# Performance work log

Hardware: AMD Instinct MI355X
Metric: run time of the kernel (lower is better)

The kernel has to match this reference:

```python
import jax, jax.numpy as jnp
import numpy as np

L_MAX = 5
C_IN = 24
HIDDEN = 32
BATCH = 256


def _valid_pairs(l):
    return [(l1, l2) for l1 in range(L_MAX + 1) for l2 in range(L_MAX + 1)
            if abs(l1 - l2) <= l <= l1 + l2]


def _make_cg():
    # Packed padded CG coefficient tensor cg[l1, l2, l, m, m1, m2].
    # Values are fixed deterministic constants; sparsity follows the true
    # selection rule m = m1 + m2 (indices stored shifted by +l).
    D = 2 * L_MAX + 1
    rng = np.random.RandomState(42)
    cg = np.zeros((L_MAX + 1, L_MAX + 1, L_MAX + 1, D, D, D), dtype=np.float32)
    for l in range(L_MAX + 1):
        for (l1, l2) in _valid_pairs(l):
            m = np.arange(-l, l + 1)[:, None, None]
            m1 = np.arange(-l1, l1 + 1)[None, :, None]
            m2 = np.arange(-l2, l2 + 1)[None, None, :]
            mask = (m == m1 + m2).astype(np.float32)
            vals = rng.randn(2 * l + 1, 2 * l1 + 1, 2 * l2 + 1).astype(np.float32)
            cg[l1, l2, l, :2 * l + 1, :2 * l1 + 1, :2 * l2 + 1] = vals * mask
    return jnp.asarray(cg)


def setup_inputs() -> dict:
    key = jax.random.key(0)
    keys = jax.random.split(key, 12)
    inp = {}
    for l in range(L_MAX + 1):
        inp[f"x{l}"] = jax.random.normal(keys[l], (BATCH, C_IN, 2 * l + 1), dtype=jnp.float32)
    for l in range(L_MAX + 1):
        k_in = len(_valid_pairs(l)) * C_IN * C_IN
        scale = 1.0 / np.sqrt(k_in)
        inp[f"W{l}"] = jax.random.normal(keys[6 + l], (HIDDEN, k_in), dtype=jnp.float32) * scale
    inp["cg"] = _make_cg()
    return inp


def reference(x0, x1, x2, x3, x4, x5, W0, W1, W2, W3, W4, W5, cg):
    xs = [x0, x1, x2, x3, x4, x5]
    Ws = [W0, W1, W2, W3, W4, W5]
    outs = []
    for l in range(L_MAX + 1):
        feats = []
        for (l1, l2) in _valid_pairs(l):
            c = cg[l1, l2, l, :2 * l + 1, :2 * l1 + 1, :2 * l2 + 1]  # [2l+1, 2l1+1, 2l2+1]
            # P[b, c1, c2, m] = sum_{m1,m2} cg[m,m1,m2] x_l1[b,c1,m1] x_l2[b,c2,m2]
            p = jnp.einsum('mij,bci,bdj->bcdm', c, xs[l1], xs[l2])
            feats.append(p.reshape(p.shape[0], -1, 2 * l + 1))
        cat = jnp.concatenate(feats, axis=1)  # [B, n_pairs*C*C, 2l+1]
        outs.append(jnp.einsum('hk,bkm->bhm', Ws[l], cat))  # [B, HIDDEN, 2l+1]
    # concat orders along the m axis -> [B, HIDDEN, sum_l (2l+1) = 36]
    return jnp.concatenate(outs, axis=-1)
```

## Files before the change

kernel.cpp:

```cpp
#include <hip/hip_runtime.h>
#include <hip/hip_bf16.h>

typedef __attribute__((ext_vector_type(8))) short bf16x8;
typedef __attribute__((ext_vector_type(4))) float f32x4;
typedef __attribute__((ext_vector_type(2))) float f32x2;

struct Params {
  const float* x[6];
  const float* W[6];
  const float* cg;
  float* out;
  unsigned short* Wb;
};

constexpr int NPAIRS_C[6] = {6, 15, 21, 24, 24, 21};
constexpr int POFF_C[6]   = {0, 6, 21, 42, 66, 90};
constexpr size_t WBASE_C[6] = {0, 110592, 387072, 774144, 1216512, 1658880};
constexpr int KL_C[6]   = {3456, 8640, 12096, 13824, 13824, 12096};
constexpr int LOFF_C[6] = {0, 1, 4, 9, 16, 25};

constexpr int TL1[111] = {
  0,1,2,3,4,5,
  0,1,1,1,2,2,2,3,3,3,4,4,4,5,5,
  0,1,1,1,2,2,2,2,2,3,3,3,3,3,4,4,4,4,5,5,5,
  0,1,1,1,2,2,2,2,2,3,3,3,3,3,3,4,4,4,4,4,5,5,5,5,
  0,1,1,1,2,2,2,2,3,3,3,3,3,4,4,4,4,4,4,5,5,5,5,5,
  0,1,1,2,2,2,3,3,3,3,4,4,4,4,4,5,5,5,5,5,5
};
constexpr int TL2R[111] = {
  0,1,2,3,4,5,
  1,0,1,2,1,2,3,2,3,4,3,4,5,4,5,
  2,1,2,3,0,1,2,3,4,1,2,3,4,5,2,3,4,5,3,4,5,
  3,2,3,4,1,2,3,4,5,0,1,2,3,4,5,1,2,3,4,5,2,3,4,5,
  4,3,4,5,2,3,4,5,1,2,3,4,5,0,1,2,3,4,5,1,2,3,4,5,
  5,4,5,3,4,5,2,3,4,5,1,2,3,4,5,0,1,2,3,4,5
};

__constant__ int c_l1[111] = {
  0,1,2,3,4,5,
  0,1,1,1,2,2,2,3,3,3,4,4,4,5,5,
  0,1,1,1,2,2,2,2,2,3,3,3,3,3,4,4,4,4,5,5,5,
  0,1,1,1,2,2,2,2,2,3,3,3,3,3,3,4,4,4,4,4,5,5,5,5,
  0,1,1,1,2,2,2,2,3,3,3,3,3,4,4,4,4,4,4,5,5,5,5,5,
  0,1,1,2,2,2,3,3,3,3,4,4,4,4,4,5,5,5,5,5,5
};
__constant__ int c_l2[111] = {
  0,1,2,3,4,5,
  1,0,1,2,1,2,3,2,3,4,3,4,5,4,5,
  2,1,2,3,0,1,2,3,4,1,2,3,4,5,2,3,4,5,3,4,5,
  3,2,3,4,1,2,3,4,5,0,1,2,3,4,5,1,2,3,4,5,2,3,4,5,
  4,3,4,5,2,3,4,5,1,2,3,4,5,0,1,2,3,4,5,1,2,3,4,5,
  5,4,5,3,4,5,2,3,4,5,1,2,3,4,5,0,1,2,3,4,5
};
__constant__ int c_mb_l[21]  = {5,5,5,5,5,5, 4,4,4,4,4, 3,3,3,3, 2,2,2, 1,1, 0};
__constant__ int c_mb_m0[21] = {0,2,4,6,8,10, 0,2,4,6,8, 0,2,4,6, 0,2,4, 0,2, 0};
__constant__ int c_GA[9] = {0,1,2,6,7,8,12,13,14};

template<int L>
__device__ __forceinline__ void swz(const Params& P, int u8) {
  constexpr int KL = KL_C[L];
  constexpr int KL8 = KL / 8;
  if (u8 >= 32 * KL8) return;
  const int h  = u8 / KL8;
  const int k  = (u8 - h * KL8) * 8;
  const int pair = k / 576;
  const int kin  = k - pair * 576;
  const int kc = kin >> 5;
  const int g  = (kin >> 3) & 3;
  const float* src = P.W[L] + (size_t)h * KL + k;
  f32x4 v0 = *(const f32x4*)src;
  f32x4 v1 = *(const f32x4*)(src + 4);
  union { __hip_bfloat162 h2; unsigned int u; } z;
  unsigned int o0, o1, o2, o3;
  z.h2 = __float22bfloat162_rn(make_float2(v0.x, v0.y)); o0 = z.u;
  z.h2 = __float22bfloat162_rn(make_float2(v0.z, v0.w)); o1 = z.u;
  z.h2 = __float22bfloat162_rn(make_float2(v1.x, v1.y)); o2 = z.u;
  z.h2 = __float22bfloat162_rn(make_float2(v1.z, v1.w)); o3 = z.u;
  const size_t dst = WBASE_C[L] + (size_t)pair * 18432 + kc * 1024 + (h >> 4) * 512
                   + ((size_t)(g * 16 + (h & 15))) * 8;
  *(uint4*)(P.Wb + dst) = make_uint4(o0, o1, o2, o3);
}

__global__ __launch_bounds__(256)
void swizzle_W(Params P) {
  const int u8 = blockIdx.x * 256 + threadIdx.x;
  switch (blockIdx.y) {
    case 0: swz<0>(P, u8); break;
    case 1: swz<1>(P, u8); break;
    case 2: swz<2>(P, u8); break;
    case 3: swz<3>(P, u8); break;
    case 4: swz<4>(P, u8); break;
    default: swz<5>(P, u8); break;
  }
}

#define XALL_F 0
#define CG_F   7056
#define RED_F  7632
#define SMEM_FLOATS 9680

template<int L>
__device__ __forceinline__ void body(const Params& P, const int mp0, const int btile) {
  constexpr int NP  = NPAIRS_C[L];
  constexpr int OFF = POFF_C[L];
  extern __shared__ float smem[];
  float* xall  = smem + XALL_F;
  float* cgall = smem + CG_F;
  float* red   = smem + RED_F;

  const int t    = threadIdx.x;
  const int lane = t & 63;
  const int w    = t >> 6;
  const int q8   = lane >> 4;
  const int rI   = lane & 15;
  const int b    = rI & 7;
  const int mpL  = rI >> 3;
  const int b0   = btile * 8;

#pragma unroll
  for (int l = 0; l < 6; ++l) {
    const int n = 2 * l + 1;
    const float* src = P.x[l] + (size_t)b0 * 24 * n;
    const int tot = 8 * 24 * n;
    for (int e = t; e < tot; e += 256) {
      const int bc = e / n;
      const int i  = e - bc * n;
      xall[(LOFF_C[l] + i) * 196 + bc] = src[e];
    }
  }
  for (int e = t; e < 2 * NP * 12; e += 256) {
    const int i  = e % 12;
    const int r  = e / 12;
    const int pi = r % NP;
    const int mL = r / NP;
    const int l1 = c_l1[OFF + pi], l2 = c_l2[OFF + pi];
    const int mp = mp0 + mL;
    const int j  = mp + l1 + l2 - L - i;
    float v = 0.f;
    if (mp <= 2 * L && i <= 2 * l1 && j >= 0 && j <= 2 * l2)
      v = P.cg[((size_t)(((l1 * 6 + l2) * 6 + L) * 11 + mp) * 11 + i) * 11 + j];
    cgall[(mL * NP + pi) * 12 + i] = v;
  }
  __syncthreads();

  f32x4 accC0 = {0.f, 0.f, 0.f, 0.f};
  f32x4 accC1 = {0.f, 0.f, 0.f, 0.f};
  const int colb = b * 24;

  for (int g = w; g < 9; g += 4) {
    const int kcA = c_GA[g];
    const int k0  = kcA * 32 + q8 * 8;
    const int cA  = k0 / 24;
    const int d0  = k0 - cA * 24;
    const float* x2base = xall + colb + d0;
    const float* x1base = xall + colb + cA;

#pragma unroll
    for (int pi = 0; pi < NP; ++pi) {
      constexpr int dummy = 0; (void)dummy;
      const int l1 = TL1[OFF + pi], l2 = TL2R[OFF + pi];
      const int n1 = 2 * l1 + 1, n2 = 2 * l2 + 1;
      const int R1 = LOFF_C[l1], R2 = LOFF_C[l2];
      const int mK0w = mp0 + l1 + l2 - L;
      const int mK0l = mK0w + mpL;
      const int i0 = (mK0w - (n2 - 1)) > 0 ? (mK0w - (n2 - 1)) : 0;
      const int i1 = (n1 - 1) < (mK0w + 1) ? (n1 - 1) : (mK0w + 1);

      const unsigned short* wbp = P.Wb + WBASE_C[L] + (size_t)pi * 18432 + lane * 8;
      const bf16x8 wfA0 = *(const bf16x8*)(wbp + kcA * 1024);
      const bf16x8 wfA1 = *(const bf16x8*)(wbp + kcA * 1024 + 512);
      const bf16x8 wfB0 = *(const bf16x8*)(wbp + (kcA + 3) * 1024);
      const bf16x8 wfB1 = *(const bf16x8*)(wbp + (kcA + 3) * 1024 + 512);

      f32x2 pA[4], pB[4];
#pragma unroll
      for (int dd = 0; dd < 4; ++dd) { pA[dd] = (f32x2){0.f, 0.f}; pB[dd] = (f32x2){0.f, 0.f}; }

      const float* cgp = cgall + (mpL * NP + pi) * 12;
      for (int i = i0; i <= i1; ++i) {
        const float cgv = cgp[i];
        int j = mK0l - i;
        j = j < 0 ? 0 : (j > n2 - 1 ? n2 - 1 : j);
        const float* x2p = x2base + (R2 + j) * 196;
        f32x2 xv[4];
        *(f32x4*)&xv[0] = *(const f32x4*)x2p;
        *(f32x4*)&xv[2] = *(const f32x4*)(x2p + 4);
        const float* x1p = x1base + (R1 + i) * 196;
        const float sA = cgv * x1p[0];
        const float sB = cgv * x1p[4];
        const f32x2 svA = {sA, sA}, svB = {sB, sB};
#pragma unroll
        for (int dd = 0; dd < 4; ++dd) {
          pA[dd] += svA * xv[dd];
          pB[dd] += svB * xv[dd];
        }
      }
      union { unsigned int u[4]; bf16x8 v; } zA, zB;
#pragma unroll
      for (int dd = 0; dd < 4; ++dd) {
        union { __hip_bfloat162 h2; unsigned int u; } z;
        z.h2 = __float22bfloat162_rn(make_float2(pA[dd].x, pA[dd].y)); zA.u[dd] = z.u;
        z.h2 = __float22bfloat162_rn(make_float2(pB[dd].x, pB[dd].y)); zB.u[dd] = z.u;
      }
      accC0 = __builtin_amdgcn_mfma_f32_16x16x32_bf16(zA.v, wfA0, accC0, 0, 0, 0);
      accC0 = __builtin_amdgcn_mfma_f32_16x16x32_bf16(zB.v, wfB0, accC0, 0, 0, 0);
      accC1 = __builtin_amdgcn_mfma_f32_16x16x32_bf16(zA.v, wfA1, accC1, 0, 0, 0);
      accC1 = __builtin_amdgcn_mfma_f32_16x16x32_bf16(zB.v, wfB1, accC1, 0, 0, 0);
    }
  }

  {
    const int col16 = lane & 15;
    const int rbase = (w * 16 + (lane >> 4) * 4);
#pragma unroll
    for (int r = 0; r < 4; ++r) {
      red[(rbase + r) * 32 + col16]      = accC0[r];
      red[(rbase + r) * 32 + 16 + col16] = accC1[r];
    }
  }
  __syncthreads();
#pragma unroll
  for (int it = 0; it < 2; ++it) {
    const int idx = t + 256 * it;
    const int row = idx >> 5, h = idx & 31;
    const float v = red[row * 32 + h] + red[512 + row * 32 + h]
                  + red[1024 + row * 32 + h] + red[1536 + row * 32 + h];
    const int ob = row & 7, omL = row >> 3;
    const int mp = mp0 + omL;
    if (mp <= 2 * L)
      P.out[(size_t)(b0 + ob) * 1152 + h * 36 + L * L + mp] = v;
  }
}

__global__ __launch_bounds__(256, 4)
void CGLayer_main(Params P) {
  const int mb = blockIdx.x;
  const int l = c_mb_l[mb], mp0 = c_mb_m0[mb];
  const int btile = blockIdx.y;
  switch (l) {
    case 0: body<0>(P, mp0, btile); break;
    case 1: body<1>(P, mp0, btile); break;
    case 2: body<2>(P, mp0, btile); break;
    case 3: body<3>(P, mp0, btile); break;
    case 4: body<4>(P, mp0, btile); break;
    default: body<5>(P, mp0, btile); break;
  }
}

extern "C" void kernel_launch(void* const* d_in, const int* in_sizes, int n_in,
                              void* d_out, int out_size, void* d_ws, size_t ws_size,
                              hipStream_t stream) {
  Params P;
  for (int i = 0; i < 6; ++i) P.x[i] = (const float*)d_in[i];
  for (int i = 0; i < 6; ++i) P.W[i] = (const float*)d_in[6 + i];
  P.cg  = (const float*)d_in[12];
  P.out = (float*)d_out;
  P.Wb  = (unsigned short*)d_ws;

  dim3 sg(216, 6);
  swizzle_W<<<sg, 256, 0, stream>>>(P);
  dim3 grid(21, 32);
  CGLayer_main<<<grid, 256, SMEM_FLOATS * sizeof(float), stream>>>(P);
}
```

Measured before the change: 168.3 us.

## Drop W swizzle kernel, convert fp32 weights inline, use 9 waves per block

Removes the separate swizzle kernel that converted W to a bf16 MFMA-friendly layout in workspace. The main kernel now reads fp32 W directly from the input and converts it to bf16 in registers before each MFMA. Blocks grow to 576 threads, so each of the 9 k-chunk groups gets its own wave instead of 4 waves looping over them, and the reduction sums over 9 partial buffers. This saves one launch and the workspace write/read, but doubles weight load bytes per MFMA and adds conversion work in the hot loop. The larger reduction buffer also raises shared memory per block.

```diff
diff --git a/kernel.cpp b/kernel.cpp
--- a/kernel.cpp
+++ b/kernel.cpp
@@ -10,12 +10,10 @@
   const float* W[6];
   const float* cg;
   float* out;
-  unsigned short* Wb;
 };
 
 constexpr int NPAIRS_C[6] = {6, 15, 21, 24, 24, 21};
 constexpr int POFF_C[6]   = {0, 6, 21, 42, 66, 90};
-constexpr size_t WBASE_C[6] = {0, 110592, 387072, 774144, 1216512, 1658880};
 constexpr int KL_C[6]   = {3456, 8640, 12096, 13824, 13824, 12096};
 constexpr int LOFF_C[6] = {0, 1, 4, 9, 16, 25};
 
@@ -56,53 +54,26 @@
 __constant__ int c_mb_m0[21] = {0,2,4,6,8,10, 0,2,4,6,8, 0,2,4,6, 0,2,4, 0,2, 0};
 __constant__ int c_GA[9] = {0,1,2,6,7,8,12,13,14};
 
-template<int L>
-__device__ __forceinline__ void swz(const Params& P, int u8) {
-  constexpr int KL = KL_C[L];
-  constexpr int KL8 = KL / 8;
-  if (u8 >= 32 * KL8) return;
-  const int h  = u8 / KL8;
-  const int k  = (u8 - h * KL8) * 8;
-  const int pair = k / 576;
-  const int kin  = k - pair * 576;
-  const int kc = kin >> 5;
-  const int g  = (kin >> 3) & 3;
-  const float* src = P.W[L] + (size_t)h * KL + k;
-  f32x4 v0 = *(const f32x4*)src;
-  f32x4 v1 = *(const f32x4*)(src + 4);
-  union { __hip_bfloat162 h2; unsigned int u; } z;
-  unsigned int o0, o1, o2, o3;
-  z.h2 = __float22bfloat162_rn(make_float2(v0.x, v0.y)); o0 = z.u;
-  z.h2 = __float22bfloat162_rn(make_float2(v0.z, v0.w)); o1 = z.u;
-  z.h2 = __float22bfloat162_rn(make_float2(v1.x, v1.y)); o2 = z.u;
-  z.h2 = __float22bfloat162_rn(make_float2(v1.z, v1.w)); o3 = z.u;
-  const size_t dst = WBASE_C[L] + (size_t)pair * 18432 + kc * 1024 + (h >> 4) * 512
-                   + ((size_t)(g * 16 + (h & 15))) * 8;
-  *(uint4*)(P.Wb + dst) = make_uint4(o0, o1, o2, o3);
-}
-
-__global__ __launch_bounds__(256)
-void swizzle_W(Params P) {
-  const int u8 = blockIdx.x * 256 + threadIdx.x;
-  switch (blockIdx.y) {
-    case 0: swz<0>(P, u8); break;
-    case 1: swz<1>(P, u8); break;
-    case 2: swz<2>(P, u8); break;
-    case 3: swz<3>(P, u8); break;
-    case 4: swz<4>(P, u8); break;
-    default: swz<5>(P, u8); break;
-  }
-}
-
 #define XALL_F 0
 #define CG_F   7056
 #define RED_F  7632
-#define SMEM_FLOATS 9680
+#define SMEM_FLOATS 12240
+
+__device__ __forceinline__ bf16x8 cvt8(f32x4 lo, f32x4 hi) {
+  union { unsigned int u[4]; bf16x8 v; } z;
+  union { __hip_bfloat162 h2; unsigned int u; } y;
+  y.h2 = __float22bfloat162_rn(make_float2(lo.x, lo.y)); z.u[0] = y.u;
+  y.h2 = __float22bfloat162_rn(make_float2(lo.z, lo.w)); z.u[1] = y.u;
+  y.h2 = __float22bfloat162_rn(make_float2(hi.x, hi.y)); z.u[2] = y.u;
+  y.h2 = __float22bfloat162_rn(make_float2(hi.z, hi.w)); z.u[3] = y.u;
+  return z.v;
+}
 
 template<int L>
 __device__ __forceinline__ void body(const Params& P, const int mp0, const int btile) {
   constexpr int NP  = NPAIRS_C[L];
   constexpr int OFF = POFF_C[L];
+  constexpr int KL  = KL_C[L];
   extern __shared__ float smem[];
   float* xall  = smem + XALL_F;
   float* cgall = smem + CG_F;
@@ -122,13 +93,13 @@
     const int n = 2 * l + 1;
     const float* src = P.x[l] + (size_t)b0 * 24 * n;
     const int tot = 8 * 24 * n;
-    for (int e = t; e < tot; e += 256) {
+    for (int e = t; e < tot; e += 576) {
       const int bc = e / n;
       const int i  = e - bc * n;
       xall[(LOFF_C[l] + i) * 196 + bc] = src[e];
     }
   }
-  for (int e = t; e < 2 * NP * 12; e += 256) {
+  for (int e = t; e < 2 * NP * 12; e += 576) {
     const int i  = e % 12;
     const int r  = e / 12;
     const int pi = r % NP;
@@ -147,71 +118,80 @@
   f32x4 accC1 = {0.f, 0.f, 0.f, 0.f};
   const int colb = b * 24;
 
-  for (int g = w; g < 9; g += 4) {
-    const int kcA = c_GA[g];
-    const int k0  = kcA * 32 + q8 * 8;
-    const int cA  = k0 / 24;
-    const int d0  = k0 - cA * 24;
-    const float* x2base = xall + colb + d0;
-    const float* x1base = xall + colb + cA;
-
-#pragma unroll
-    for (int pi = 0; pi < NP; ++pi) {
-      constexpr int dummy = 0; (void)dummy;
-      const int l1 = TL1[OFF + pi], l2 = TL2R[OFF + pi];
-      const int n1 = 2 * l1 + 1, n2 = 2 * l2 + 1;
-      const int R1 = LOFF_C[l1], R2 = LOFF_C[l2];
-      const int mK0w = mp0 + l1 + l2 - L;
-      const int mK0l = mK0w + mpL;
-      const int i0 = (mK0w - (n2 - 1)) > 0 ? (mK0w - (n2 - 1)) : 0;
-      const int i1 = (n1 - 1) < (mK0w + 1) ? (n1 - 1) : (mK0w + 1);
-
-      const unsigned short* wbp = P.Wb + WBASE_C[L] + (size_t)pi * 18432 + lane * 8;
-      const bf16x8 wfA0 = *(const bf16x8*)(wbp + kcA * 1024);
-      const bf16x8 wfA1 = *(const bf16x8*)(wbp + kcA * 1024 + 512);
-      const bf16x8 wfB0 = *(const bf16x8*)(wbp + (kcA + 3) * 1024);
-      const bf16x8 wfB1 = *(const bf16x8*)(wbp + (kcA + 3) * 1024 + 512);
-
-      f32x2 pA[4], pB[4];
-#pragma unroll
-      for (int dd = 0; dd < 4; ++dd) { pA[dd] = (f32x2){0.f, 0.f}; pB[dd] = (f32x2){0.f, 0.f}; }
-
-      const float* cgp = cgall + (mpL * NP + pi) * 12;
-      for (int i = i0; i <= i1; ++i) {
-        const float cgv = cgp[i];
-        int j = mK0l - i;
-        j = j < 0 ? 0 : (j > n2 - 1 ? n2 - 1 : j);
-        const float* x2p = x2base + (R2 + j) * 196;
-        f32x2 xv[4];
-        *(f32x4*)&xv[0] = *(const f32x4*)x2p;
-        *(f32x4*)&xv[2] = *(const f32x4*)(x2p + 4);
-        const float* x1p = x1base + (R1 + i) * 196;
-        const float sA = cgv * x1p[0];
-        const float sB = cgv * x1p[4];
-        const f32x2 svA = {sA, sA}, svB = {sB, sB};
-#pragma unroll
-        for (int dd = 0; dd < 4; ++dd) {
-          pA[dd] += svA * xv[dd];
-          pB[dd] += svB * xv[dd];
-        }
+  const int kcA = c_GA[w];
+  const int k0  = kcA * 32 + q8 * 8;
+  const int cA  = k0 / 24;
+  const int d0  = k0 - cA * 24;
+  const float* x2base = xall + colb + d0;
+  const float* x1base = xall + colb + cA;
+
+  const float* rowA = P.W[L] + (size_t)(lane & 15) * KL + k0;
+  const float* rowB = rowA + (size_t)16 * KL;
+
+#pragma unroll
+  for (int pi = 0; pi < NP; ++pi) {
+    const int l1 = TL1[OFF + pi], l2 = TL2R[OFF + pi];
+    const int n1 = 2 * l1 + 1, n2 = 2 * l2 + 1;
+    const int R1 = LOFF_C[l1], R2 = LOFF_C[l2];
+    const int mK0w = mp0 + l1 + l2 - L;
+    const int mK0l = mK0w + mpL;
+    const int i0 = (mK0w - (n2 - 1)) > 0 ? (mK0w - (n2 - 1)) : 0;
+    const int i1 = (n1 - 1) < (mK0w + 1) ? (n1 - 1) : (mK0w + 1);
+
+    const float* wpA = rowA + pi * 576;
+    const float* wpB = rowB + pi * 576;
+    const f32x4 wA0lo = *(const f32x4*)(wpA);
+    const f32x4 wA0hi = *(const f32x4*)(wpA + 4);
+    const f32x4 wA1lo = *(const f32x4*)(wpB);
+    const f32x4 wA1hi = *(const f32x4*)(wpB + 4);
+    const f32x4 wB0lo = *(const f32x4*)(wpA + 96);
+    const f32x4 wB0hi = *(const f32x4*)(wpA + 100);
+    const f32x4 wB1lo = *(const f32x4*)(wpB + 96);
+    const f32x4 wB1hi = *(const f32x4*)(wpB + 100);
+
+    f32x2 pA[4], pB[4];
+#pragma unroll
+    for (int dd = 0; dd < 4; ++dd) { pA[dd] = (f32x2){0.f, 0.f}; pB[dd] = (f32x2){0.f, 0.f}; }
+
+    const float* cgp = cgall + (mpL * NP + pi) * 12;
+    for (int i = i0; i <= i1; ++i) {
+      const float cgv = cgp[i];
+      int j = mK0l - i;
+      j = j < 0 ? 0 : (j > n2 - 1 ? n2 - 1 : j);
+      const float* x2p = x2base + (R2 + j) * 196;
+      f32x2 xv[4];
+      *(f32x4*)&xv[0] = *(const f32x4*)x2p;
+      *(f32x4*)&xv[2] = *(const f32x4*)(x2p + 4);
+      const float* x1p = x1base + (R1 + i) * 196;
+      const float sA = cgv * x1p[0];
+      const float sB = cgv * x1p[4];
+      const f32x2 svA = {sA, sA}, svB = {sB, sB};
+#pragma unroll
+      for (int dd = 0; dd < 4; ++dd) {
+        pA[dd] += svA * xv[dd];
+        pB[dd] += svB * xv[dd];
       }
-      union { unsigned int u[4]; bf16x8 v; } zA, zB;
-#pragma unroll
-      for (int dd = 0; dd < 4; ++dd) {
-        union { __hip_bfloat162 h2; unsigned int u; } z;
-        z.h2 = __float22bfloat162_rn(make_float2(pA[dd].x, pA[dd].y)); zA.u[dd] = z.u;
-        z.h2 = __float22bfloat162_rn(make_float2(pB[dd].x, pB[dd].y)); zB.u[dd] = z.u;
-      }
-      accC0 = __builtin_amdgcn_mfma_f32_16x16x32_bf16(zA.v, wfA0, accC0, 0, 0, 0);
-      accC0 = __builtin_amdgcn_mfma_f32_16x16x32_bf16(zB.v, wfB0, accC0, 0, 0, 0);
-      accC1 = __builtin_amdgcn_mfma_f32_16x16x32_bf16(zA.v, wfA1, accC1, 0, 0, 0);
-      accC1 = __builtin_amdgcn_mfma_f32_16x16x32_bf16(zB.v, wfB1, accC1, 0, 0, 0);
-    }
+    }
+    union { unsigned int u[4]; bf16x8 v; } zA, zB;
+#pragma unroll
+    for (int dd = 0; dd < 4; ++dd) {
+      union { __hip_bfloat162 h2; unsigned int u; } z;
+      z.h2 = __float22bfloat162_rn(make_float2(pA[dd].x, pA[dd].y)); zA.u[dd] = z.u;
+      z.h2 = __float22bfloat162_rn(make_float2(pB[dd].x, pB[dd].y)); zB.u[dd] = z.u;
+    }
+    const bf16x8 wfA0 = cvt8(wA0lo, wA0hi);
+    const bf16x8 wfA1 = cvt8(wA1lo, wA1hi);
+    const bf16x8 wfB0 = cvt8(wB0lo, wB0hi);
+    const bf16x8 wfB1 = cvt8(wB1lo, wB1hi);
+    accC0 = __builtin_amdgcn_mfma_f32_16x16x32_bf16(zA.v, wfA0, accC0, 0, 0, 0);
+    accC0 = __builtin_amdgcn_mfma_f32_16x16x32_bf16(zB.v, wfB0, accC0, 0, 0, 0);
+    accC1 = __builtin_amdgcn_mfma_f32_16x16x32_bf16(zA.v, wfA1, accC1, 0, 0, 0);
+    accC1 = __builtin_amdgcn_mfma_f32_16x16x32_bf16(zB.v, wfB1, accC1, 0, 0, 0);
   }
 
   {
     const int col16 = lane & 15;
-    const int rbase = (w * 16 + (lane >> 4) * 4);
+    const int rbase = w * 16 + (lane >> 4) * 4;
 #pragma unroll
     for (int r = 0; r < 4; ++r) {
       red[(rbase + r) * 32 + col16]      = accC0[r];
@@ -219,12 +199,11 @@
     }
   }
   __syncthreads();
-#pragma unroll
-  for (int it = 0; it < 2; ++it) {
-    const int idx = t + 256 * it;
-    const int row = idx >> 5, h = idx & 31;
-    const float v = red[row * 32 + h] + red[512 + row * 32 + h]
-                  + red[1024 + row * 32 + h] + red[1536 + row * 32 + h];
+  if (t < 512) {
+    const int row = t >> 5, h = t & 31;
+    float v = 0.f;
+#pragma unroll
+    for (int ww = 0; ww < 9; ++ww) v += red[ww * 512 + row * 32 + h];
     const int ob = row & 7, omL = row >> 3;
     const int mp = mp0 + omL;
     if (mp <= 2 * L)
@@ -232,7 +211,7 @@
   }
 }
 
-__global__ __launch_bounds__(256, 4)
+__global__ __launch_bounds__(576, 5)
 void CGLayer_main(Params P) {
   const int mb = blockIdx.x;
   const int l = c_mb_l[mb], mp0 = c_mb_m0[mb];
@@ -255,10 +234,7 @@
   for (int i = 0; i < 6; ++i) P.W[i] = (const float*)d_in[6 + i];
   P.cg  = (const float*)d_in[12];
   P.out = (float*)d_out;
-  P.Wb  = (unsigned short*)d_ws;
-
-  dim3 sg(216, 6);
-  swizzle_W<<<sg, 256, 0, stream>>>(P);
+
   dim3 grid(21, 32);
-  CGLayer_main<<<grid, 256, SMEM_FLOATS * sizeof(float), stream>>>(P);
-}
+  CGLayer_main<<<grid, 576, SMEM_FLOATS * sizeof(float), stream>>>(P);
+}
```

Result: slower. 245.0 us (+45.6%).

## Use six waves per block with three K-chunks each instead of four imbalanced waves

Applied to the files above, without the earlier changes.

The main kernel goes from 256 to 384 threads, so six waves each own one fixed group of three K-chunks. This replaces the old loop where four waves shared nine chunk groups unevenly, leaving one wave with three groups while the others had two. Each wave now builds three A fragments per pair, reusing the x2 loads across them, and issues six MFMAs per pair. The x tile row stride is padded from 196 to 204, and the reduction sums six partial buffers. This raises shared memory use and register pressure per thread.

```diff
diff --git a/kernel.cpp b/kernel.cpp
--- a/kernel.cpp
+++ b/kernel.cpp
@@ -18,6 +18,7 @@
 constexpr size_t WBASE_C[6] = {0, 110592, 387072, 774144, 1216512, 1658880};
 constexpr int KL_C[6]   = {3456, 8640, 12096, 13824, 13824, 12096};
 constexpr int LOFF_C[6] = {0, 1, 4, 9, 16, 25};
+#define XSTRIDE 204
 
 constexpr int TL1[111] = {
   0,1,2,3,4,5,
@@ -54,7 +55,7 @@
 };
 __constant__ int c_mb_l[21]  = {5,5,5,5,5,5, 4,4,4,4,4, 3,3,3,3, 2,2,2, 1,1, 0};
 __constant__ int c_mb_m0[21] = {0,2,4,6,8,10, 0,2,4,6,8, 0,2,4,6, 0,2,4, 0,2, 0};
-__constant__ int c_GA[9] = {0,1,2,6,7,8,12,13,14};
+__constant__ int c_GA3[6] = {0,1,2,9,10,11};
 
 template<int L>
 __device__ __forceinline__ void swz(const Params& P, int u8) {
@@ -95,9 +96,9 @@
 }
 
 #define XALL_F 0
-#define CG_F   7056
-#define RED_F  7632
-#define SMEM_FLOATS 9680
+#define CG_F   7344
+#define RED_F  7920
+#define SMEM_FLOATS 10992
 
 template<int L>
 __device__ __forceinline__ void body(const Params& P, const int mp0, const int btile) {
@@ -122,13 +123,13 @@
     const int n = 2 * l + 1;
     const float* src = P.x[l] + (size_t)b0 * 24 * n;
     const int tot = 8 * 24 * n;
-    for (int e = t; e < tot; e += 256) {
+    for (int e = t; e < tot; e += 384) {
       const int bc = e / n;
       const int i  = e - bc * n;
-      xall[(LOFF_C[l] + i) * 196 + bc] = src[e];
-    }
-  }
-  for (int e = t; e < 2 * NP * 12; e += 256) {
+      xall[(LOFF_C[l] + i) * XSTRIDE + bc] = src[e];
+    }
+  }
+  for (int e = t; e < 2 * NP * 12; e += 384) {
     const int i  = e % 12;
     const int r  = e / 12;
     const int pi = r % NP;
@@ -147,71 +148,79 @@
   f32x4 accC1 = {0.f, 0.f, 0.f, 0.f};
   const int colb = b * 24;
 
-  for (int g = w; g < 9; g += 4) {
-    const int kcA = c_GA[g];
-    const int k0  = kcA * 32 + q8 * 8;
-    const int cA  = k0 / 24;
-    const int d0  = k0 - cA * 24;
-    const float* x2base = xall + colb + d0;
-    const float* x1base = xall + colb + cA;
-
-#pragma unroll
-    for (int pi = 0; pi < NP; ++pi) {
-      constexpr int dummy = 0; (void)dummy;
-      const int l1 = TL1[OFF + pi], l2 = TL2R[OFF + pi];
-      const int n1 = 2 * l1 + 1, n2 = 2 * l2 + 1;
-      const int R1 = LOFF_C[l1], R2 = LOFF_C[l2];
-      const int mK0w = mp0 + l1 + l2 - L;
-      const int mK0l = mK0w + mpL;
-      const int i0 = (mK0w - (n2 - 1)) > 0 ? (mK0w - (n2 - 1)) : 0;
-      const int i1 = (n1 - 1) < (mK0w + 1) ? (n1 - 1) : (mK0w + 1);
-
-      const unsigned short* wbp = P.Wb + WBASE_C[L] + (size_t)pi * 18432 + lane * 8;
-      const bf16x8 wfA0 = *(const bf16x8*)(wbp + kcA * 1024);
-      const bf16x8 wfA1 = *(const bf16x8*)(wbp + kcA * 1024 + 512);
-      const bf16x8 wfB0 = *(const bf16x8*)(wbp + (kcA + 3) * 1024);
-      const bf16x8 wfB1 = *(const bf16x8*)(wbp + (kcA + 3) * 1024 + 512);
-
-      f32x2 pA[4], pB[4];
-#pragma unroll
-      for (int dd = 0; dd < 4; ++dd) { pA[dd] = (f32x2){0.f, 0.f}; pB[dd] = (f32x2){0.f, 0.f}; }
-
-      const float* cgp = cgall + (mpL * NP + pi) * 12;
-      for (int i = i0; i <= i1; ++i) {
-        const float cgv = cgp[i];
-        int j = mK0l - i;
-        j = j < 0 ? 0 : (j > n2 - 1 ? n2 - 1 : j);
-        const float* x2p = x2base + (R2 + j) * 196;
-        f32x2 xv[4];
-        *(f32x4*)&xv[0] = *(const f32x4*)x2p;
-        *(f32x4*)&xv[2] = *(const f32x4*)(x2p + 4);
-        const float* x1p = x1base + (R1 + i) * 196;
-        const float sA = cgv * x1p[0];
-        const float sB = cgv * x1p[4];
-        const f32x2 svA = {sA, sA}, svB = {sB, sB};
-#pragma unroll
-        for (int dd = 0; dd < 4; ++dd) {
-          pA[dd] += svA * xv[dd];
-          pB[dd] += svB * xv[dd];
-        }
+  const int kcA = c_GA3[w];
+  const int k0  = kcA * 32 + q8 * 8;
+  const int cA  = k0 / 24;
+  const int d0  = k0 - cA * 24;
+  const float* x2base = xall + colb + d0;
+  const float* x1base = xall + colb + cA;
+
+#pragma unroll
+  for (int pi = 0; pi < NP; ++pi) {
+    const int l1 = TL1[OFF + pi], l2 = TL2R[OFF + pi];
+    const int n1 = 2 * l1 + 1, n2 = 2 * l2 + 1;
+    const int R1 = LOFF_C[l1], R2 = LOFF_C[l2];
+    const int mK0w = mp0 + l1 + l2 - L;
+    const int mK0l = mK0w + mpL;
+    const int i0 = (mK0w - (n2 - 1)) > 0 ? (mK0w - (n2 - 1)) : 0;
+    const int i1 = (n1 - 1) < (mK0w + 1) ? (n1 - 1) : (mK0w + 1);
+
+    const unsigned short* wbp = P.Wb + WBASE_C[L] + (size_t)pi * 18432 + lane * 8;
+    const bf16x8 wfA0 = *(const bf16x8*)(wbp + kcA * 1024);
+    const bf16x8 wfA1 = *(const bf16x8*)(wbp + kcA * 1024 + 512);
+    const bf16x8 wfB0 = *(const bf16x8*)(wbp + (kcA + 3) * 1024);
+    const bf16x8 wfB1 = *(const bf16x8*)(wbp + (kcA + 3) * 1024 + 512);
+    const bf16x8 wfC0 = *(const bf16x8*)(wbp + (kcA + 6) * 1024);
+    const bf16x8 wfC1 = *(const bf16x8*)(wbp + (kcA + 6) * 1024 + 512);
+
+    f32x2 pA[4], pB[4], pC[4];
+#pragma unroll
+    for (int dd = 0; dd < 4; ++dd) {
+      pA[dd] = (f32x2){0.f, 0.f};
+      pB[dd] = (f32x2){0.f, 0.f};
+      pC[dd] = (f32x2){0.f, 0.f};
+    }
+
+    const float* cgp = cgall + (mpL * NP + pi) * 12;
+    for (int i = i0; i <= i1; ++i) {
+      const float cgv = cgp[i];
+      int j = mK0l - i;
+      j = j < 0 ? 0 : (j > n2 - 1 ? n2 - 1 : j);
+      const float* x2p = x2base + (R2 + j) * XSTRIDE;
+      f32x2 xv[4];
+      *(f32x4*)&xv[0] = *(const f32x4*)x2p;
+      *(f32x4*)&xv[2] = *(const f32x4*)(x2p + 4);
+      const float* x1p = x1base + (R1 + i) * XSTRIDE;
+      const float sA = cgv * x1p[0];
+      const float sB = cgv * x1p[4];
+      const float sC = cgv * x1p[8];
+      const f32x2 svA = {sA, sA}, svB = {sB, sB}, svC = {sC, sC};
+#pragma unroll
+      for (int dd = 0; dd < 4; ++dd) {
+        pA[dd] += svA * xv[dd];
+        pB[dd] += svB * xv[dd];
+        pC[dd] += svC * xv[dd];
       }
-      union { unsigned int u[4]; bf16x8 v; } zA, zB;
-#pragma unroll
-      for (int dd = 0; dd < 4; ++dd) {
-        union { __hip_bfloat162 h2; unsigned int u; } z;
-        z.h2 = __float22bfloat162_rn(make_float2(pA[dd].x, pA[dd].y)); zA.u[dd] = z.u;
-        z.h2 = __float22bfloat162_rn(make_float2(pB[dd].x, pB[dd].y)); zB.u[dd] = z.u;
-      }
-      accC0 = __builtin_amdgcn_mfma_f32_16x16x32_bf16(zA.v, wfA0, accC0, 0, 0, 0);
-      accC0 = __builtin_amdgcn_mfma_f32_16x16x32_bf16(zB.v, wfB0, accC0, 0, 0, 0);
-      accC1 = __builtin_amdgcn_mfma_f32_16x16x32_bf16(zA.v, wfA1, accC1, 0, 0, 0);
-      accC1 = __builtin_amdgcn_mfma_f32_16x16x32_bf16(zB.v, wfB1, accC1, 0, 0, 0);
-    }
+    }
+    union { unsigned int u[4]; bf16x8 v; } zA, zB, zC;
+#pragma unroll
+    for (int dd = 0; dd < 4; ++dd) {
+      union { __hip_bfloat162 h2; unsigned int u; } z;
+      z.h2 = __float22bfloat162_rn(make_float2(pA[dd].x, pA[dd].y)); zA.u[dd] = z.u;
+      z.h2 = __float22bfloat162_rn(make_float2(pB[dd].x, pB[dd].y)); zB.u[dd] = z.u;
+      z.h2 = __float22bfloat162_rn(make_float2(pC[dd].x, pC[dd].y)); zC.u[dd] = z.u;
+    }
+    accC0 = __builtin_amdgcn_mfma_f32_16x16x32_bf16(zA.v, wfA0, accC0, 0, 0, 0);
+    accC0 = __builtin_amdgcn_mfma_f32_16x16x32_bf16(zB.v, wfB0, accC0, 0, 0, 0);
+    accC0 = __builtin_amdgcn_mfma_f32_16x16x32_bf16(zC.v, wfC0, accC0, 0, 0, 0);
+    accC1 = __builtin_amdgcn_mfma_f32_16x16x32_bf16(zA.v, wfA1, accC1, 0, 0, 0);
+    accC1 = __builtin_amdgcn_mfma_f32_16x16x32_bf16(zB.v, wfB1, accC1, 0, 0, 0);
+    accC1 = __builtin_amdgcn_mfma_f32_16x16x32_bf16(zC.v, wfC1, accC1, 0, 0, 0);
   }
 
   {
     const int col16 = lane & 15;
-    const int rbase = (w * 16 + (lane >> 4) * 4);
+    const int rbase = w * 16 + (lane >> 4) * 4;
 #pragma unroll
     for (int r = 0; r < 4; ++r) {
       red[(rbase + r) * 32 + col16]      = accC0[r];
@@ -219,12 +228,11 @@
     }
   }
   __syncthreads();
-#pragma unroll
-  for (int it = 0; it < 2; ++it) {
-    const int idx = t + 256 * it;
+  for (int idx = t; idx < 512; idx += 384) {
     const int row = idx >> 5, h = idx & 31;
-    const float v = red[row * 32 + h] + red[512 + row * 32 + h]
-                  + red[1024 + row * 32 + h] + red[1536 + row * 32 + h];
+    float v = 0.f;
+#pragma unroll
+    for (int ww = 0; ww < 6; ++ww) v += red[ww * 512 + row * 32 + h];
     const int ob = row & 7, omL = row >> 3;
     const int mp = mp0 + omL;
     if (mp <= 2 * L)
@@ -232,7 +240,7 @@
   }
 }
 
-__global__ __launch_bounds__(256, 4)
+__global__ __launch_bounds__(384, 5)
 void CGLayer_main(Params P) {
   const int mb = blockIdx.x;
   const int l = c_mb_l[mb], mp0 = c_mb_m0[mb];
@@ -260,5 +268,5 @@
   dim3 sg(216, 6);
   swizzle_W<<<sg, 256, 0, stream>>>(P);
   dim3 grid(21, 32);
-  CGLayer_main<<<grid, 256, SMEM_FLOATS * sizeof(float), stream>>>(P);
-}
+  CGLayer_main<<<grid, 384, SMEM_FLOATS * sizeof(float), stream>>>(P);
+}
```

Measured after the change: 149.0 us. 11.4% less time.
